# Performance work log

Measured on AMD Instinct MI355X. Metric: run time of the kernel, lower is better.

The kernel has to match this reference:

```python
import jax, jax.numpy as jnp
import numpy as np

N_QUBITS = 4
N_FEATURES = 16
BATCH = 1048576  # 2**20

# Pauli-Z sign table: ZSIGNS[q, i] = +1 if bit of qubit q in basis index i is 0 else -1.
# Qubit q lives on axis q+1 of the (B,2,2,2,2) statevector, i.e. bit (3-q) of the flat index.
_idx = np.arange(16)
ZSIGNS = np.stack([1.0 - 2.0 * ((_idx >> (N_QUBITS - 1 - q)) & 1) for q in range(N_QUBITS)]).astype(np.float32)  # (4,16)


def _apply_1q_batched(psi, G, q):
    # psi: (B,2,2,2,2) complex, G: (B,2,2) complex, acts on qubit q (axis q+1)
    psi = jnp.moveaxis(psi, q + 1, 1)
    psi = jnp.einsum('bij,bj...->bi...', G, psi)
    return jnp.moveaxis(psi, 1, q + 1)


def _apply_1q_shared(psi, G, q):
    # G: (2,2) complex shared across batch
    psi = jnp.moveaxis(psi, q + 1, 1)
    psi = jnp.einsum('ij,bj...->bi...', G, psi)
    return jnp.moveaxis(psi, 1, q + 1)


def _apply_cnot(psi, c, t):
    # flip target axis where control bit == 1
    psi = jnp.moveaxis(psi, (c + 1, t + 1), (1, 2))
    psi = jnp.concatenate([psi[:, :1], psi[:, 1:, ::-1]], axis=1)
    return jnp.moveaxis(psi, (1, 2), (c + 1, t + 1))


def _quantum_encoder(x, q_weights):
    # x: (B,16) float32, q_weights: (8,) float32 -> (B,4) PauliZ expvals
    B = x.shape[0]
    angles = x.reshape(B, N_QUBITS, 4).mean(-1) * jnp.pi  # (B,4)
    psi = jnp.zeros((B, 16), jnp.complex64).at[:, 0].set(1.0).reshape(B, 2, 2, 2, 2)
    # data-encoding RY(angle_q) on each qubit (per-sample gates)
    ch, sh = jnp.cos(angles * 0.5), jnp.sin(angles * 0.5)
    for q in range(N_QUBITS):
        G = jnp.stack([jnp.stack([ch[:, q], -sh[:, q]], -1),
                       jnp.stack([sh[:, q], ch[:, q]], -1)], -2).astype(jnp.complex64)  # (B,2,2)
        psi = _apply_1q_batched(psi, G, q)
    # entangling CNOT chain
    for q in range(N_QUBITS - 1):
        psi = _apply_cnot(psi, q, q + 1)
    # trainable RY(w[2q]) then RZ(w[2q+1]) per qubit, fused into one 2x2 gate
    for q in range(N_QUBITS):
        ry, rz = q_weights[2 * q], q_weights[2 * q + 1]
        cr, sr = jnp.cos(ry * 0.5), jnp.sin(ry * 0.5)
        zero = jnp.zeros((), jnp.complex64)
        RY = jnp.stack([jnp.stack([cr, -sr]), jnp.stack([sr, cr])]).astype(jnp.complex64)
        e0, e1 = jnp.exp(-0.5j * rz), jnp.exp(0.5j * rz)
        RZ = jnp.stack([jnp.stack([e0.astype(jnp.complex64), zero]),
                        jnp.stack([zero, e1.astype(jnp.complex64)])])
        psi = _apply_1q_shared(psi, RZ @ RY, q)
    probs = jnp.real(psi * jnp.conj(psi)).reshape(B, 16)  # (B,16)
    return probs @ jnp.asarray(ZSIGNS).T  # (B,4)


def setup_inputs() -> dict:
    key = jax.random.key(0)
    ks = jax.random.split(key, 8)
    x = jax.random.normal(ks[0], (BATCH, N_FEATURES), jnp.float32)
    q_weights = jax.random.normal(ks[1], (2 * N_QUBITS,), jnp.float32) * 0.1
    W1 = jax.random.normal(ks[2], (16, 4), jnp.float32) * (1.0 / np.sqrt(4.0))
    b1 = jnp.zeros((16,), jnp.float32)
    W2 = jax.random.normal(ks[3], (32, 16), jnp.float32) * (1.0 / np.sqrt(16.0))
    b2 = jnp.zeros((32,), jnp.float32)
    W3 = jax.random.normal(ks[4], (16, 32), jnp.float32) * (1.0 / np.sqrt(32.0))
    b3 = jnp.zeros((16,), jnp.float32)
    return {"x": x, "q_weights": q_weights, "W1": W1, "b1": b1, "W2": W2, "b2": b2, "W3": W3, "b3": b3}


def reference(x, q_weights, W1, b1, W2, b2, W3, b3):
    z = _quantum_encoder(x, q_weights)           # (B,4)
    h = jax.nn.relu(z @ W1.T + b1)               # (B,16)
    h = jax.nn.relu(h @ W2.T + b2)               # (B,32)
    return h @ W3.T + b3                         # (B,16)
```

## Files before the change

### kernel.cpp

```cpp
#include <hip/hip_runtime.h>


typedef _Float16 f16x8 __attribute__((ext_vector_type(8)));
typedef _Float16 f16x4 __attribute__((ext_vector_type(4)));
typedef float    f32x4 __attribute__((ext_vector_type(4)));
typedef int      i32x4 __attribute__((ext_vector_type(4)));

__device__ __forceinline__ int2 pack4(float a, float b, float c, float d) {
    f16x4 v = { (_Float16)a, (_Float16)b, (_Float16)c, (_Float16)d };
    return *reinterpret_cast<int2*>(&v);
}
__device__ __forceinline__ f16x8 frag_from(int a, int b, int c, int d) {
    i32x4 v = { a, b, c, d };
    return *reinterpret_cast<f16x8*>(&v);
}

__global__ __launch_bounds__(256) void hqae_kernel(
    const float* __restrict__ x,
    const float* __restrict__ qw,
    const float* __restrict__ W1, const float* __restrict__ b1,
    const float* __restrict__ W2, const float* __restrict__ b2,
    const float* __restrict__ W3, const float* __restrict__ b3,
    float* __restrict__ out)
{
    __shared__ alignas(16) f16x8 sW1h[16];
    __shared__ alignas(16) f16x8 sW2h[64];
    __shared__ alignas(16) f16x8 sW3h[64];
    __shared__ alignas(16) float sb1[16];
    __shared__ alignas(16) float sb2[32];
    __shared__ alignas(16) float sb3[16];
    __shared__ float scw[4], ssw[4];

    const int tid = threadIdx.x;
    _Float16* w1p = (_Float16*)sW1h;
    _Float16* w2p = (_Float16*)sW2h;
    _Float16* w3p = (_Float16*)sW3h;
    for (int t = tid; t < 512; t += 256) {
        w2p[t] = (_Float16)W2[t];
        w3p[t] = (_Float16)W3[t];
    }
    if (tid < 128) w1p[tid] = ((tid & 7) < 4) ? (_Float16)W1[(tid >> 3) * 4 + (tid & 7)]
                                              : (_Float16)0.f;
    if (tid < 16) { sb1[tid] = b1[tid]; sb3[tid] = b3[tid]; }
    if (tid < 32) sb2[tid] = b2[tid];
    if (tid < 4)  { float a = qw[2 * tid]; scw[tid] = __cosf(a); ssw[tid] = __sinf(a); }
    __syncthreads();

    const int wv   = tid >> 6;
    const int lane = tid & 63;
    const int g    = lane >> 4;
    const int ln15 = lane & 15;
    const int base = blockIdx.x * 256 + wv * 64;

    int2 dz;
    {
        const float4* xin = reinterpret_cast<const float4*>(x + (size_t)(base + lane) * 16);
        float4 a0 = xin[0], a1 = xin[1], a2 = xin[2], a3 = xin[3];
        const float PI4 = 0.78539816339744831f;
        float t0 = (a0.x + a0.y + a0.z + a0.w) * PI4;
        float t1 = (a1.x + a1.y + a1.z + a1.w) * PI4;
        float t2 = (a2.x + a2.y + a2.z + a2.w) * PI4;
        float t3 = (a3.x + a3.y + a3.z + a3.w) * PI4;
        float C0 = __cosf(t0), S0 = __sinf(t0);
        float C1 = __cosf(t1), S1 = __sinf(t1);
        float C2 = __cosf(t2), S2 = __sinf(t2);
        float C3 = __cosf(t3), S3 = __sinf(t3);
        float C01 = C0 * C1, C012 = C01 * C2, C0123 = C012 * C3;
        float z0 = scw[0] * C0    - ssw[0] * (S0 * S1);
        float z1 = scw[1] * C01   - ssw[1] * (S1 * S2);
        float z2 = scw[2] * C012  - ssw[2] * (S2 * S3);
        float z3 = scw[3] * C0123 - ssw[3] * S3;
        dz = pack4(z0, z1, z2, z3);
    }

    f16x8 aW1   = sW1h[ln15];
    f32x4 bias1 = ((const f32x4*)sb1)[g];
    const int gh = g & 1;
    f16x8 aW2_0 = sW2h[(0 * 16 + ln15) * 2 + gh];
    f16x8 aW2_1 = sW2h[(1 * 16 + ln15) * 2 + gh];
    f32x4 bias2_0 = ((const f32x4*)sb2)[g];
    f32x4 bias2_1 = ((const f32x4*)sb2)[4 + g];
    f16x8 aW3   = sW3h[ln15 * 4 + g];
    f32x4 bias3 = ((const f32x4*)sb3)[g];

    const int sA = ((g & 1) << 5) + ln15;
    const int sB = sA + 16;

#pragma unroll
    for (int st = 0; st < 4; ++st) {
        int src = st * 16 + ln15;
        int zlo = __shfl(dz.x, src), zhi = __shfl(dz.y, src);
        f16x8 bf1 = (g == 0) ? frag_from(zlo, zhi, 0, 0) : (f16x8)0;
        f32x4 d1 = __builtin_amdgcn_mfma_f32_16x16x32_f16(aW1, bf1, bias1, 0, 0, 0);
        int2 h1 = pack4(fmaxf(d1[0], 0.f), fmaxf(d1[1], 0.f),
                        fmaxf(d1[2], 0.f), fmaxf(d1[3], 0.f));

        int b0 = __shfl(h1.x, sA), b1v = __shfl(h1.y, sA);
        int b2v = __shfl(h1.x, sB), b3v = __shfl(h1.y, sB);
        f16x8 bf2 = (g < 2) ? frag_from(b0, b1v, b2v, b3v) : (f16x8)0;
        f32x4 d2a = __builtin_amdgcn_mfma_f32_16x16x32_f16(aW2_0, bf2, bias2_0, 0, 0, 0);
        f32x4 d2b = __builtin_amdgcn_mfma_f32_16x16x32_f16(aW2_1, bf2, bias2_1, 0, 0, 0);
        int2 h2a = pack4(fmaxf(d2a[0], 0.f), fmaxf(d2a[1], 0.f),
                         fmaxf(d2a[2], 0.f), fmaxf(d2a[3], 0.f));
        int2 h2b = pack4(fmaxf(d2b[0], 0.f), fmaxf(d2b[1], 0.f),
                         fmaxf(d2b[2], 0.f), fmaxf(d2b[3], 0.f));

        int a0 = __shfl(h2a.x, sA), a1 = __shfl(h2a.y, sA);
        int a2 = __shfl(h2a.x, sB), a3 = __shfl(h2a.y, sB);
        int c0 = __shfl(h2b.x, sA), c1 = __shfl(h2b.y, sA);
        int c2 = __shfl(h2b.x, sB), c3 = __shfl(h2b.y, sB);
        f16x8 bf3 = (g < 2) ? frag_from(a0, a1, a2, a3)
                            : frag_from(c0, c1, c2, c3);
        f32x4 d3 = __builtin_amdgcn_mfma_f32_16x16x32_f16(aW3, bf3, bias3, 0, 0, 0);

        f32x4* op = reinterpret_cast<f32x4*>(out + (size_t)(base + st * 16 + ln15) * 16 + g * 4);
        __builtin_nontemporal_store(d3, op);
    }
}

extern "C" void kernel_launch(void* const* d_in, const int* in_sizes, int n_in,
                              void* d_out, int out_size, void* d_ws, size_t ws_size,
                              hipStream_t stream) {
    const float* x  = (const float*)d_in[0];
    const float* qw = (const float*)d_in[1];
    const float* W1 = (const float*)d_in[2];
    const float* b1 = (const float*)d_in[3];
    const float* W2 = (const float*)d_in[4];
    const float* b2 = (const float*)d_in[5];
    const float* W3 = (const float*)d_in[6];
    const float* b3 = (const float*)d_in[7];
    float* out = (float*)d_out;

    const int B = in_sizes[0] / 16;
    hqae_kernel<<<B / 256, 256, 0, stream>>>(x, qw, W1, b1, W2, b2, W3, b3, out);
}
```

Baseline: 26.91 us.

## Process four tiles per block with register prefetch of next input tile

Each block now handles four 256-row tiles, strided by the grid size, instead of one, and the launch uses a quarter as many blocks. This amortises the per-block shared-memory weight staging and sync across more rows. While computing the current tile, the next tile's input rows are loaded into registers so global load latency overlaps with the MFMA work. The cost is more registers per thread and fewer blocks, which may reduce occupancy and latency hiding.

Result: slower. 27.93 us (+3.8%).

```diff
diff --git a/kernel.cpp b/kernel.cpp
--- a/kernel.cpp
+++ b/kernel.cpp
@@ -5,6 +5,8 @@
 typedef _Float16 f16x4 __attribute__((ext_vector_type(4)));
 typedef float    f32x4 __attribute__((ext_vector_type(4)));
 typedef int      i32x4 __attribute__((ext_vector_type(4)));
+
+#define TPB 4
 
 __device__ __forceinline__ int2 pack4(float a, float b, float c, float d) {
     f16x4 v = { (_Float16)a, (_Float16)b, (_Float16)c, (_Float16)d };
@@ -50,28 +52,6 @@
     const int lane = tid & 63;
     const int g    = lane >> 4;
     const int ln15 = lane & 15;
-    const int base = blockIdx.x * 256 + wv * 64;
-
-    int2 dz;
-    {
-        const float4* xin = reinterpret_cast<const float4*>(x + (size_t)(base + lane) * 16);
-        float4 a0 = xin[0], a1 = xin[1], a2 = xin[2], a3 = xin[3];
-        const float PI4 = 0.78539816339744831f;
-        float t0 = (a0.x + a0.y + a0.z + a0.w) * PI4;
-        float t1 = (a1.x + a1.y + a1.z + a1.w) * PI4;
-        float t2 = (a2.x + a2.y + a2.z + a2.w) * PI4;
-        float t3 = (a3.x + a3.y + a3.z + a3.w) * PI4;
-        float C0 = __cosf(t0), S0 = __sinf(t0);
-        float C1 = __cosf(t1), S1 = __sinf(t1);
-        float C2 = __cosf(t2), S2 = __sinf(t2);
-        float C3 = __cosf(t3), S3 = __sinf(t3);
-        float C01 = C0 * C1, C012 = C01 * C2, C0123 = C012 * C3;
-        float z0 = scw[0] * C0    - ssw[0] * (S0 * S1);
-        float z1 = scw[1] * C01   - ssw[1] * (S1 * S2);
-        float z2 = scw[2] * C012  - ssw[2] * (S2 * S3);
-        float z3 = scw[3] * C0123 - ssw[3] * S3;
-        dz = pack4(z0, z1, z2, z3);
-    }
 
     f16x8 aW1   = sW1h[ln15];
     f32x4 bias1 = ((const f32x4*)sb1)[g];
@@ -83,38 +63,83 @@
     f16x8 aW3   = sW3h[ln15 * 4 + g];
     f32x4 bias3 = ((const f32x4*)sb3)[g];
 
+    const float kq0 = scw[0], kq1 = scw[1], kq2 = scw[2], kq3 = scw[3];
+    const float lq0 = ssw[0], lq1 = ssw[1], lq2 = ssw[2], lq3 = ssw[3];
+
     const int sA = ((g & 1) << 5) + ln15;
     const int sB = sA + 16;
 
+    const int stride = gridDim.x;
+
+    f32x4 cur0, cur1, cur2, cur3;
+    {
+        const int base = (blockIdx.x) * 256 + wv * 64;
+        const f32x4* xin = reinterpret_cast<const f32x4*>(x + (size_t)(base + lane) * 16);
+        cur0 = xin[0]; cur1 = xin[1]; cur2 = xin[2]; cur3 = xin[3];
+    }
+
 #pragma unroll
-    for (int st = 0; st < 4; ++st) {
-        int src = st * 16 + ln15;
-        int zlo = __shfl(dz.x, src), zhi = __shfl(dz.y, src);
-        f16x8 bf1 = (g == 0) ? frag_from(zlo, zhi, 0, 0) : (f16x8)0;
-        f32x4 d1 = __builtin_amdgcn_mfma_f32_16x16x32_f16(aW1, bf1, bias1, 0, 0, 0);
-        int2 h1 = pack4(fmaxf(d1[0], 0.f), fmaxf(d1[1], 0.f),
-                        fmaxf(d1[2], 0.f), fmaxf(d1[3], 0.f));
+    for (int k = 0; k < TPB; ++k) {
+        const int base = (blockIdx.x + k * stride) * 256 + wv * 64;
 
-        int b0 = __shfl(h1.x, sA), b1v = __shfl(h1.y, sA);
-        int b2v = __shfl(h1.x, sB), b3v = __shfl(h1.y, sB);
-        f16x8 bf2 = (g < 2) ? frag_from(b0, b1v, b2v, b3v) : (f16x8)0;
-        f32x4 d2a = __builtin_amdgcn_mfma_f32_16x16x32_f16(aW2_0, bf2, bias2_0, 0, 0, 0);
-        f32x4 d2b = __builtin_amdgcn_mfma_f32_16x16x32_f16(aW2_1, bf2, bias2_1, 0, 0, 0);
-        int2 h2a = pack4(fmaxf(d2a[0], 0.f), fmaxf(d2a[1], 0.f),
-                         fmaxf(d2a[2], 0.f), fmaxf(d2a[3], 0.f));
-        int2 h2b = pack4(fmaxf(d2b[0], 0.f), fmaxf(d2b[1], 0.f),
-                         fmaxf(d2b[2], 0.f), fmaxf(d2b[3], 0.f));
+        f32x4 nxt0, nxt1, nxt2, nxt3;
+        if (k + 1 < TPB) {
+            const int nbase = (blockIdx.x + (k + 1) * stride) * 256 + wv * 64;
+            const f32x4* xin = reinterpret_cast<const f32x4*>(x + (size_t)(nbase + lane) * 16);
+            nxt0 = xin[0]; nxt1 = xin[1]; nxt2 = xin[2]; nxt3 = xin[3];
+        }
 
-        int a0 = __shfl(h2a.x, sA), a1 = __shfl(h2a.y, sA);
-        int a2 = __shfl(h2a.x, sB), a3 = __shfl(h2a.y, sB);
-        int c0 = __shfl(h2b.x, sA), c1 = __shfl(h2b.y, sA);
-        int c2 = __shfl(h2b.x, sB), c3 = __shfl(h2b.y, sB);
-        f16x8 bf3 = (g < 2) ? frag_from(a0, a1, a2, a3)
-                            : frag_from(c0, c1, c2, c3);
-        f32x4 d3 = __builtin_amdgcn_mfma_f32_16x16x32_f16(aW3, bf3, bias3, 0, 0, 0);
+        int2 dz;
+        {
+            const float PI4 = 0.78539816339744831f;
+            float t0 = (cur0[0] + cur0[1] + cur0[2] + cur0[3]) * PI4;
+            float t1 = (cur1[0] + cur1[1] + cur1[2] + cur1[3]) * PI4;
+            float t2 = (cur2[0] + cur2[1] + cur2[2] + cur2[3]) * PI4;
+            float t3 = (cur3[0] + cur3[1] + cur3[2] + cur3[3]) * PI4;
+            float C0 = __cosf(t0), S0 = __sinf(t0);
+            float C1 = __cosf(t1), S1 = __sinf(t1);
+            float C2 = __cosf(t2), S2 = __sinf(t2);
+            float C3 = __cosf(t3), S3 = __sinf(t3);
+            float C01 = C0 * C1, C012 = C01 * C2, C0123 = C012 * C3;
+            float z0 = kq0 * C0    - lq0 * (S0 * S1);
+            float z1 = kq1 * C01   - lq1 * (S1 * S2);
+            float z2 = kq2 * C012  - lq2 * (S2 * S3);
+            float z3 = kq3 * C0123 - lq3 * S3;
+            dz = pack4(z0, z1, z2, z3);
+        }
 
-        f32x4* op = reinterpret_cast<f32x4*>(out + (size_t)(base + st * 16 + ln15) * 16 + g * 4);
-        __builtin_nontemporal_store(d3, op);
+#pragma unroll
+        for (int st = 0; st < 4; ++st) {
+            int src = st * 16 + ln15;
+            int zlo = __shfl(dz.x, src), zhi = __shfl(dz.y, src);
+            f16x8 bf1 = (g == 0) ? frag_from(zlo, zhi, 0, 0) : (f16x8)0;
+            f32x4 d1 = __builtin_amdgcn_mfma_f32_16x16x32_f16(aW1, bf1, bias1, 0, 0, 0);
+            int2 h1 = pack4(fmaxf(d1[0], 0.f), fmaxf(d1[1], 0.f),
+                            fmaxf(d1[2], 0.f), fmaxf(d1[3], 0.f));
+
+            int b0 = __shfl(h1.x, sA), b1v = __shfl(h1.y, sA);
+            int b2v = __shfl(h1.x, sB), b3v = __shfl(h1.y, sB);
+            f16x8 bf2 = (g < 2) ? frag_from(b0, b1v, b2v, b3v) : (f16x8)0;
+            f32x4 d2a = __builtin_amdgcn_mfma_f32_16x16x32_f16(aW2_0, bf2, bias2_0, 0, 0, 0);
+            f32x4 d2b = __builtin_amdgcn_mfma_f32_16x16x32_f16(aW2_1, bf2, bias2_1, 0, 0, 0);
+            int2 h2a = pack4(fmaxf(d2a[0], 0.f), fmaxf(d2a[1], 0.f),
+                             fmaxf(d2a[2], 0.f), fmaxf(d2a[3], 0.f));
+            int2 h2b = pack4(fmaxf(d2b[0], 0.f), fmaxf(d2b[1], 0.f),
+                             fmaxf(d2b[2], 0.f), fmaxf(d2b[3], 0.f));
+
+            int a0 = __shfl(h2a.x, sA), a1 = __shfl(h2a.y, sA);
+            int a2 = __shfl(h2a.x, sB), a3 = __shfl(h2a.y, sB);
+            int c0 = __shfl(h2b.x, sA), c1 = __shfl(h2b.y, sA);
+            int c2 = __shfl(h2b.x, sB), c3 = __shfl(h2b.y, sB);
+            f16x8 bf3 = (g < 2) ? frag_from(a0, a1, a2, a3)
+                                : frag_from(c0, c1, c2, c3);
+            f32x4 d3 = __builtin_amdgcn_mfma_f32_16x16x32_f16(aW3, bf3, bias3, 0, 0, 0);
+
+            f32x4* op = reinterpret_cast<f32x4*>(out + (size_t)(base + st * 16 + ln15) * 16 + g * 4);
+            __builtin_nontemporal_store(d3, op);
+        }
+
+        cur0 = nxt0; cur1 = nxt1; cur2 = nxt2; cur3 = nxt3;
     }
 }
 
@@ -132,5 +157,6 @@
     float* out = (float*)d_out;
 
     const int B = in_sizes[0] / 16;
-    hqae_kernel<<<B / 256, 256, 0, stream>>>(x, qw, W1, b1, W2, b2, W3, b3, out);
+    const int grid = B / (256 * TPB);
+    hqae_kernel<<<grid, 256, 0, stream>>>(x, qw, W1, b1, W2, b2, W3, b3, out);
 }
```
